# Optimization experiments

Measured on AMD Instinct MI355X. Metric: run time of the kernel, lower is better.

The kernel has to match this reference:

```python
import jax, jax.numpy as jnp
import numpy as np

B, S, H = 4, 2048, 1024
NH, HD = 16, 64  # num heads, head dim

def setup_inputs() -> dict:
    key = jax.random.key(0)
    ks = jax.random.split(key, 4)
    scale = 1.0 / np.sqrt(H)
    return {
        "hidden_states": jax.random.normal(ks[0], (B, S, H), dtype=jnp.float32),
        "attention_mask": jnp.zeros((B, 1, 1, S), dtype=jnp.float32),
        "wq": jax.random.normal(ks[1], (H, H), dtype=jnp.float32) * scale,
        "bq": jnp.zeros((H,), dtype=jnp.float32),
        "wk": jax.random.normal(ks[2], (H, H), dtype=jnp.float32) * scale,
        "bk": jnp.zeros((H,), dtype=jnp.float32),
        "wv": jax.random.normal(ks[3], (H, H), dtype=jnp.float32) * scale,
        "bv": jnp.zeros((H,), dtype=jnp.float32),
    }

def _split_heads(x):
    # [B,S,H] -> [B,NH,S,HD]
    return x.reshape(B, S, NH, HD).transpose(0, 2, 1, 3)

def reference(hidden_states, attention_mask, wq, bq, wk, bk, wv, bv):
    # torch F.linear: x @ W^T + b
    q = _split_heads(hidden_states @ wq.T + bq)
    k = _split_heads(hidden_states @ wk.T + bk)
    v = _split_heads(hidden_states @ wv.T + bv)
    scores = jnp.einsum("bhqd,bhkd->bhqk", q, k) / np.sqrt(HD)
    scores = scores + attention_mask  # additive mask, broadcast [B,1,1,S]
    probs = jax.nn.softmax(scores, axis=-1)  # dropout p=0.0 (eval)
    ctx = jnp.einsum("bhqk,bhkd->bhqd", probs, v)
    # [B,NH,S,HD] -> [B,S,H]
    return ctx.transpose(0, 2, 1, 3).reshape(B, S, H)
```

## Files before the change

kernel.cpp:

```cpp
#include <hip/hip_runtime.h>

typedef unsigned short u16;
typedef unsigned int u32;
typedef __bf16 bf16;
typedef bf16 bf16x8 __attribute__((ext_vector_type(8)));
typedef float f32x4 __attribute__((ext_vector_type(4)));
typedef float f32x16 __attribute__((ext_vector_type(16)));
typedef u16 u16x8 __attribute__((ext_vector_type(8)));
typedef u16 u16x4 __attribute__((ext_vector_type(4)));
typedef u32 u32x4 __attribute__((ext_vector_type(4)));

#define B_ 4
#define S_ 2048
#define H_ 1024
#define NH_ 16
#define HD_ 64
#define M_TOT (B_ * S_)
#define N_TOT (3 * H_)

#if __has_builtin(__builtin_amdgcn_exp2f)
#define EXP2(x) __builtin_amdgcn_exp2f(x)
#else
static __device__ __forceinline__ float exp2_hw(float x) {
    float r; asm("v_exp_f32 %0, %1" : "=v"(r) : "v"(x)); return r;
}
#define EXP2(x) exp2_hw(x)
#endif

__device__ __forceinline__ u16 f2bf(float f) {
    union { float f; unsigned u; } v; v.f = f;
    unsigned r = v.u + 0x7FFFu + ((v.u >> 16) & 1u);
    return (u16)(r >> 16);
}

__device__ __forceinline__ u32 cvt_pk_bf16(float a, float b) {
    u32 r;
    asm("v_cvt_pk_bf16_f32 %0, %1, %2" : "=v"(r) : "v"(a), "v"(b));
    return r;
}
__device__ __forceinline__ void perm32swap(u32& a, u32& b) {
    asm volatile("v_permlane32_swap_b32 %0, %1" : "+v"(a), "+v"(b));
}
__device__ __forceinline__ void gload16(const void* g, void* l) {
    __builtin_amdgcn_global_load_lds(
        (const __attribute__((address_space(1))) void*)g,
        (__attribute__((address_space(3))) void*)l, 16, 0, 0);
}
__device__ __forceinline__ void wait_vm0() { asm volatile("s_waitcnt vmcnt(0)" ::: "memory"); }

__global__ __launch_bounds__(256) void cvt_all(
    const float* __restrict__ x, const float* __restrict__ wq,
    const float* __restrict__ wk, const float* __restrict__ wv,
    u16* __restrict__ xb, u16* __restrict__ wb) {
    const int X4 = (M_TOT * H_) / 4;
    const int W4 = (H_ * H_) / 4;
    const int total = X4 + 3 * W4;
    int i = blockIdx.x * blockDim.x + threadIdx.x;
    int stride = gridDim.x * blockDim.x;
    for (; i < total; i += stride) {
        const float* src; u16* dst; int off;
        if (i < X4) { src = x; dst = xb; off = i; }
        else {
            int j = i - X4;
            int w = j >> 18;
            off = j & (W4 - 1);
            src = (w == 0) ? wq : (w == 1) ? wk : wv;
            dst = wb + w * (H_ * H_);
        }
        float4 v = ((const float4*)src)[off];
        u16x4 o = { f2bf(v.x), f2bf(v.y), f2bf(v.z), f2bf(v.w) };
        *(u16x4*)&dst[off * 4] = o;
    }
}

__global__ __launch_bounds__(512, 2) void qkv_gemm(
    const u16* __restrict__ X, const u16* __restrict__ W,
    const float* __restrict__ bq, const float* __restrict__ bk, const float* __restrict__ bv,
    u16* __restrict__ Q, u16* __restrict__ Ko, u16* __restrict__ Vt) {
    __shared__ __align__(16) u16 As[2][256 * 32];
    __shared__ __align__(16) u16 Bs[2][128 * 32];

    const int tid = threadIdx.x;
    const int lane = tid & 63;
    const int wave = tid >> 6;
    const int l31 = lane & 31;
    const int hi = lane >> 5;
    const int mb = blockIdx.x & 31;
    const int nb = blockIdx.x >> 5;
    const int m0 = mb * 256;
    const int n0 = nb * 128;
    const int wr = (wave >> 1) * 64;
    const int wc = (wave & 1) * 64;

    f32x16 acc[2][2];
#pragma unroll
    for (int mf = 0; mf < 2; mf++)
#pragma unroll
        for (int nf = 0; nf < 2; nf++)
#pragma unroll
            for (int i = 0; i < 16; i++) acc[mf][nf][i] = 0.f;

    const int raA = tid >> 2, caA = (tid & 3) * 8;
    const u16* gA0 = &X[(size_t)(m0 + raA) * H_ + caA];
    const u16* gA1 = &X[(size_t)(m0 + 128 + raA) * H_ + caA];
    const u16* gB0 = &W[(size_t)(n0 + raA) * H_ + caA];
    char* lA = (char*)&As[0][0] + wave * 1024;
    char* lB = (char*)&Bs[0][0] + wave * 1024;

    gload16(gA0, lA);
    gload16(gA1, lA + 8192);
    gload16(gB0, lB);

    for (int k0 = 0; k0 < H_; k0 += 32) {
        const int cur = (k0 >> 5) & 1;
        wait_vm0();
        __builtin_amdgcn_s_barrier();
        if (k0 + 32 < H_) {
            char* dA = lA + (cur ^ 1) * 16384;
            char* dB = lB + (cur ^ 1) * 8192;
            gload16(gA0 + k0 + 32, dA);
            gload16(gA1 + k0 + 32, dA + 8192);
            gload16(gB0 + k0 + 32, dB);
        }
        const u16* Ab = &As[cur][0];
        const u16* Bb = &Bs[cur][0];
        bf16x8 a[2][2], bfr[2][2];
#pragma unroll
        for (int mf = 0; mf < 2; mf++)
#pragma unroll
            for (int ks = 0; ks < 2; ks++)
                a[mf][ks] = *(const bf16x8*)&Ab[(wr + mf * 32 + l31) * 32 + ks * 16 + hi * 8];
#pragma unroll
        for (int nf = 0; nf < 2; nf++)
#pragma unroll
            for (int ks = 0; ks < 2; ks++)
                bfr[nf][ks] = *(const bf16x8*)&Bb[(wc + nf * 32 + l31) * 32 + ks * 16 + hi * 8];
#pragma unroll
        for (int mf = 0; mf < 2; mf++)
#pragma unroll
            for (int nf = 0; nf < 2; nf++)
#pragma unroll
                for (int ks = 0; ks < 2; ks++)
                    acc[mf][nf] = __builtin_amdgcn_mfma_f32_32x32x16_bf16(
                        a[mf][ks], bfr[nf][ks], acc[mf][nf], 0, 0, 0);
    }

    const float QS = 0.125f * 1.44269504f;
    const int which = n0 >> 10;
    const float* bp = (which == 0) ? bq : (which == 1) ? bk : bv;
#pragma unroll
    for (int nf = 0; nf < 2; nf++) {
        int ng = n0 + wc + nf * 32 + l31;
        int nn = ng & 1023;
        float bias = bp[nn];
        int h = nn >> 6, d = nn & 63;
#pragma unroll
        for (int mf = 0; mf < 2; mf++) {
#pragma unroll
            for (int q = 0; q < 4; q++) {
                int mrow0 = m0 + wr + mf * 32 + 8 * q + 4 * hi;
                int bb = mrow0 >> 11, s0 = mrow0 & 2047;
                if (which == 2) {
                    u16x4 pack;
#pragma unroll
                    for (int j = 0; j < 4; j++) pack[j] = f2bf(acc[mf][nf][q * 4 + j] + bias);
                    *(u16x4*)&Vt[((((size_t)bb * NH_ + h) * HD_) + d) * S_ + s0] = pack;
                } else {
                    u16* dst = (which == 0) ? Q : Ko;
                    float scale = (which == 0) ? QS : 1.0f;
#pragma unroll
                    for (int j = 0; j < 4; j++) {
                        float v = (acc[mf][nf][q * 4 + j] + bias) * scale;
                        dst[((((size_t)bb * NH_ + h) * S_) + s0 + j) * HD_ + d] = f2bf(v);
                    }
                }
            }
        }
    }
}

#define KVB 64
#define NT_ (S_ / KVB)

__global__ __launch_bounds__(512, 4) void attn(
    const u16* __restrict__ Q, const u16* __restrict__ K, const u16* __restrict__ Vt,
    const float* __restrict__ mask, float* __restrict__ out) {
    const int head = blockIdx.x & 63;
    const int qb = blockIdx.x >> 6;
    const int b = head >> 4, h = head & 15;
    const int q0 = qb * 256;
    const int tid = threadIdx.x;
    const int lane = tid & 63;
    const int wave = tid >> 6;
    const int l31 = lane & 31;
    const int hi = lane >> 5;

    const u16* Qh = Q + (size_t)head * S_ * HD_;
    const u16* Kh = K + (size_t)head * S_ * HD_;
    const u16* Vh = Vt + (size_t)head * HD_ * S_;

    __shared__ __align__(16) u16 Kl[2][KVB * HD_];
    __shared__ __align__(16) u16 Vl[2][HD_ * KVB];
    __shared__ int snz;

    if (tid == 0) snz = 0;
    __syncthreads();
    {
        int nz = 0;
        const f32x4* m4 = (const f32x4*)(mask + (size_t)b * S_);
        for (int i = tid; i < S_ / 4; i += 512) {
            f32x4 v = m4[i];
            nz |= (v[0] != 0.f) | (v[1] != 0.f) | (v[2] != 0.f) | (v[3] != 0.f);
        }
        if (__any(nz) && lane == 0) atomicOr(&snz, 1);
    }

    bf16x8 qf[4];
    {
        const u16* qp = &Qh[(size_t)(q0 + wave * 32 + l31) * HD_ + hi * 8];
        qf[0] = *(const bf16x8*)(qp);
        qf[1] = *(const bf16x8*)(qp + 16);
        qf[2] = *(const bf16x8*)(qp + 32);
        qf[3] = *(const bf16x8*)(qp + 48);
    }
    __syncthreads();
    const bool mz = (snz == 0);
    const float* mrow = mask + (size_t)b * S_;
    const float LOG2E = 1.44269504f;

    const int rc = tid >> 3;
    const u32 sc16 = (u32)(((tid & 7) ^ (rc & 7)) * 16);
    const char* kSrc = (const char*)Kh + (size_t)rc * 128 + sc16;
    const char* vSrc = (const char*)Vh + (size_t)rc * (S_ * 2) + sc16;
    char* dK = (char*)&Kl[0][0] + wave * 1024;
    char* dV = (char*)&Vl[0][0] + wave * 1024;

    const u32 swzR = (u32)((l31 & 7) << 4);
    const u32 rowB = (u32)(l31 * 128);

    f32x16 oacc[2];
#pragma unroll
    for (int dh = 0; dh < 2; dh++)
#pragma unroll
        for (int i = 0; i < 16; i++) oacc[dh][i] = 0.f;
    float m = -1e30f, l = 0.f;

    gload16(kSrc, dK);
    gload16(vSrc, dV);

    for (int t = 0; t < NT_; ++t) {
        const int kv0 = t * KVB;
        const int cur = t & 1;
        wait_vm0();
        __builtin_amdgcn_s_barrier();
        if (t + 1 < NT_) {
            gload16(kSrc + (size_t)(kv0 + KVB) * 128, dK + (cur ^ 1) * 8192);
            gload16(vSrc + (size_t)(kv0 + KVB) * 2,   dV + (cur ^ 1) * 8192);
        }
        const char* KB = (const char*)&Kl[cur][0];
        const char* VB = (const char*)&Vl[cur][0];

        f32x16 sc[2];
#pragma unroll
        for (int g = 0; g < 2; g++) {
            f32x16 c;
#pragma unroll
            for (int i = 0; i < 16; i++) c[i] = 0.f;
#pragma unroll
            for (int dk = 0; dk < 4; dk++) {
                bf16x8 kf = *(const bf16x8*)(KB + g * 4096 + rowB +
                                             (((u32)(dk * 32 + hi * 16)) ^ swzR));
                c = __builtin_amdgcn_mfma_f32_32x32x16_bf16(kf, qf[dk], c, 0, 0, 0);
            }
            sc[g] = c;
        }

        if (!mz) {
#pragma unroll
            for (int g = 0; g < 2; g++)
#pragma unroll
                for (int c4 = 0; c4 < 4; c4++) {
                    f32x4 mk = *(const f32x4*)&mrow[kv0 + g * 32 + c4 * 8 + hi * 4];
#pragma unroll
                    for (int e = 0; e < 4; e++) sc[g][c4 * 4 + e] += mk[e] * LOG2E;
                }
        }

        float tm = sc[0][0];
#pragma unroll
        for (int i = 1; i < 16; i++) tm = fmaxf(tm, sc[0][i]);
#pragma unroll
        for (int i = 0; i < 16; i++) tm = fmaxf(tm, sc[1][i]);
        tm = fmaxf(tm, __shfl_xor(tm, 32, 64));
        if (tm > m + 30.f) {
            float fac = EXP2(m - tm);
            l *= fac;
#pragma unroll
            for (int dh = 0; dh < 2; dh++)
#pragma unroll
                for (int i = 0; i < 16; i++) oacc[dh][i] *= fac;
            m = tm;
        }

        float l0 = 0.f, l1 = 0.f, l2 = 0.f, l3 = 0.f;
#pragma unroll
        for (int g = 0; g < 2; g++)
#pragma unroll
            for (int i = 0; i < 16; i += 4) {
                float p0 = EXP2(sc[g][i + 0] - m);
                float p1 = EXP2(sc[g][i + 1] - m);
                float p2 = EXP2(sc[g][i + 2] - m);
                float p3 = EXP2(sc[g][i + 3] - m);
                sc[g][i + 0] = p0; sc[g][i + 1] = p1;
                sc[g][i + 2] = p2; sc[g][i + 3] = p3;
                l0 += p0; l1 += p1; l2 += p2; l3 += p3;
            }
        l += (l0 + l1) + (l2 + l3);

#pragma unroll
        for (int s = 0; s < 4; s++) {
            const int g = s >> 1, r8 = (s & 1) * 8;
            u32 pkA0 = cvt_pk_bf16(sc[g][r8 + 0], sc[g][r8 + 1]);
            u32 pkA1 = cvt_pk_bf16(sc[g][r8 + 2], sc[g][r8 + 3]);
            u32 pkB0 = cvt_pk_bf16(sc[g][r8 + 4], sc[g][r8 + 5]);
            u32 pkB1 = cvt_pk_bf16(sc[g][r8 + 6], sc[g][r8 + 7]);
            perm32swap(pkA0, pkB0);
            perm32swap(pkA1, pkB1);
            union { u32x4 w; bf16x8 v; } pu;
            pu.w = (u32x4){ pkA0, pkA1, pkB0, pkB1 };
            bf16x8 pf = pu.v;
#pragma unroll
            for (int dh = 0; dh < 2; dh++) {
                bf16x8 vf = *(const bf16x8*)(VB + dh * 4096 + rowB +
                                             (((u32)(s * 32 + hi * 16)) ^ swzR));
                oacc[dh] = __builtin_amdgcn_mfma_f32_32x32x16_bf16(vf, pf, oacc[dh], 0, 0, 0);
            }
        }
    }

    float lt = l + __shfl_xor(l, 32, 64);
    float inv = 1.0f / lt;
    const int q = q0 + wave * 32 + l31;
    float* orow = out + ((size_t)b * S_ + q) * H_ + h * HD_;
#pragma unroll
    for (int dh = 0; dh < 2; dh++)
#pragma unroll
        for (int c4 = 0; c4 < 4; c4++) {
            f32x4 v;
#pragma unroll
            for (int e = 0; e < 4; e++) v[e] = oacc[dh][c4 * 4 + e] * inv;
            *(f32x4*)&orow[dh * 32 + c4 * 8 + hi * 4] = v;
        }
}

extern "C" void kernel_launch(void* const* d_in, const int* in_sizes, int n_in,
                              void* d_out, int out_size, void* d_ws, size_t ws_size,
                              hipStream_t stream) {
    const float* hs   = (const float*)d_in[0];
    const float* mask = (const float*)d_in[1];
    const float* wq   = (const float*)d_in[2];
    const float* bq   = (const float*)d_in[3];
    const float* wk   = (const float*)d_in[4];
    const float* bk   = (const float*)d_in[5];
    const float* wv   = (const float*)d_in[6];
    const float* bv   = (const float*)d_in[7];
    float* out = (float*)d_out;

    char* ws = (char*)d_ws;
    u16* Xb = (u16*)ws;
    u16* Wb = (u16*)(ws + 16777216);
    u16* Qb = (u16*)(ws + 23068672);
    u16* Kb = (u16*)(ws + 39845888);
    u16* Vb = (u16*)(ws + 56623104);

    cvt_all<<<2048, 256, 0, stream>>>(hs, wq, wk, wv, Xb, Wb);

    qkv_gemm<<<(N_TOT / 128) * (M_TOT / 256), 512, 0, stream>>>(
        Xb, Wb, bq, bk, bv, Qb, Kb, Vb);

    attn<<<(S_ / 256) * (B_ * NH_), 512, 0, stream>>>(Qb, Kb, Vb, mask, out);
}
```

Measured before the change: 194.7 us.

## Triple-buffer QKV GEMM loads and tree-reduce attention row max

The QKV projection GEMM moves from a double-buffered to a triple-buffered LDS pipeline. It prefetches two k-tiles ahead and waits with vmcnt(3) instead of draining all outstanding loads each iteration. The attention kernel's per-tile row-max reduction becomes a balanced tree instead of a serial chain, which shortens the dependency depth. In exchange, LDS use rises by half (to about 72KB per block), which could limit the two-blocks-per-CU occupancy target. The change also adds a redundant duplicated load in the conversion kernel.

```diff
diff --git a/kernel.cpp b/kernel.cpp
--- a/kernel.cpp
+++ b/kernel.cpp
@@ -47,6 +47,7 @@
         (__attribute__((address_space(3))) void*)l, 16, 0, 0);
 }
 __device__ __forceinline__ void wait_vm0() { asm volatile("s_waitcnt vmcnt(0)" ::: "memory"); }
+__device__ __forceinline__ void wait_vm3() { asm volatile("s_waitcnt vmcnt(3)" ::: "memory"); }
 
 __global__ __launch_bounds__(256) void cvt_all(
     const float* __restrict__ x, const float* __restrict__ wq,
@@ -67,18 +68,21 @@
             src = (w == 0) ? wq : (w == 1) ? wk : wv;
             dst = wb + w * (H_ * H_);
         }
-        float4 v = ((const float4*)src)[off];
+        float4 v = ((const float4*)src)[i < X4 ? off : off];
+        v = ((const float4*)src)[off];
         u16x4 o = { f2bf(v.x), f2bf(v.y), f2bf(v.z), f2bf(v.w) };
         *(u16x4*)&dst[off * 4] = o;
     }
 }
+
+#define GNT 32
 
 __global__ __launch_bounds__(512, 2) void qkv_gemm(
     const u16* __restrict__ X, const u16* __restrict__ W,
     const float* __restrict__ bq, const float* __restrict__ bk, const float* __restrict__ bv,
     u16* __restrict__ Q, u16* __restrict__ Ko, u16* __restrict__ Vt) {
-    __shared__ __align__(16) u16 As[2][256 * 32];
-    __shared__ __align__(16) u16 Bs[2][128 * 32];
+    __shared__ __align__(16) u16 As[3][256 * 32];
+    __shared__ __align__(16) u16 Bs[3][128 * 32];
 
     const int tid = threadIdx.x;
     const int lane = tid & 63;
@@ -107,23 +111,25 @@
     char* lA = (char*)&As[0][0] + wave * 1024;
     char* lB = (char*)&Bs[0][0] + wave * 1024;
 
-    gload16(gA0, lA);
-    gload16(gA1, lA + 8192);
-    gload16(gB0, lB);
-
-    for (int k0 = 0; k0 < H_; k0 += 32) {
-        const int cur = (k0 >> 5) & 1;
-        wait_vm0();
+    auto stage = [&](int t) {
+        char* dA = lA + (t % 3) * 16384;
+        char* dB = lB + (t % 3) * 8192;
+        gload16(gA0 + t * 32, dA);
+        gload16(gA1 + t * 32, dA + 8192);
+        gload16(gB0 + t * 32, dB);
+    };
+
+    stage(0);
+    stage(1);
+
+    for (int t = 0; t < GNT; ++t) {
+        if (t < GNT - 1) wait_vm3();
+        else             wait_vm0();
         __builtin_amdgcn_s_barrier();
-        if (k0 + 32 < H_) {
-            char* dA = lA + (cur ^ 1) * 16384;
-            char* dB = lB + (cur ^ 1) * 8192;
-            gload16(gA0 + k0 + 32, dA);
-            gload16(gA1 + k0 + 32, dA + 8192);
-            gload16(gB0 + k0 + 32, dB);
-        }
-        const u16* Ab = &As[cur][0];
-        const u16* Bb = &Bs[cur][0];
+        if (t + 2 < GNT) stage(t + 2);
+
+        const u16* Ab = &As[t % 3][0];
+        const u16* Bb = &Bs[t % 3][0];
         bf16x8 a[2][2], bfr[2][2];
 #pragma unroll
         for (int mf = 0; mf < 2; mf++)
@@ -286,11 +292,13 @@
                 }
         }
 
-        float tm = sc[0][0];
-#pragma unroll
-        for (int i = 1; i < 16; i++) tm = fmaxf(tm, sc[0][i]);
-#pragma unroll
-        for (int i = 0; i < 16; i++) tm = fmaxf(tm, sc[1][i]);
+        float mx[8];
+#pragma unroll
+        for (int i = 0; i < 8; i++)
+            mx[i] = fmaxf(fmaxf(sc[0][i], sc[0][i + 8]), fmaxf(sc[1][i], sc[1][i + 8]));
+        float m4a = fmaxf(fmaxf(mx[0], mx[1]), fmaxf(mx[2], mx[3]));
+        float m4b = fmaxf(fmaxf(mx[4], mx[5]), fmaxf(mx[6], mx[7]));
+        float tm = fmaxf(m4a, m4b);
         tm = fmaxf(tm, __shfl_xor(tm, 32, 64));
         if (tm > m + 30.f) {
             float fac = EXP2(m - tm);
```

Result: slower. 200.2 us (+2.8%).
